# Kernel optimization log

Hardware: AMD Instinct MI355X
Metric: run time of the kernel (lower is better)

Reference implementation:

```python
import jax, jax.numpy as jnp
import numpy as np

IN_C, OUT_C = 64, 64
M1, M2 = 64, 64
H, W = 512, 512


def setup_inputs() -> dict:
    key = jax.random.key(0)
    ks = jax.random.split(key, 6)
    scale = 1.0 / (IN_C * M1 * M2) ** 0.5
    x = jax.random.normal(ks[0], (IN_C, H, W), dtype=jnp.float32)
    w_real = scale * jax.random.normal(ks[1], (IN_C, OUT_C, M1, M2), dtype=jnp.float32)
    w_imag = scale * jax.random.normal(ks[2], (IN_C, OUT_C, M1, M2), dtype=jnp.float32)
    b_conv = 0.01 * jax.random.normal(ks[3], (OUT_C,), dtype=jnp.float32)
    w_skip = (1.0 / IN_C ** 0.5) * jax.random.normal(ks[4], (OUT_C, IN_C), dtype=jnp.float32)
    b_skip = 0.01 * jax.random.normal(ks[5], (OUT_C,), dtype=jnp.float32)
    return {"x": x, "w_real": w_real, "w_imag": w_imag, "b_conv": b_conv,
            "w_skip": w_skip, "b_skip": b_skip}


def reference(x, w_real, w_imag, b_conv, w_skip, b_skip):
    # --- spectral convolution branch ---
    xf = jnp.fft.rfftn(x, axes=(1, 2))              # (in, H, W//2+1) complex
    xs = xf[:, :M1, :M2]                            # keep low modes (corner truncation)
    w = w_real + 1j * w_imag                        # (in, out, M1, M2)
    yf = jnp.einsum('ixy,ioxy->oxy', xs, w)         # complex mode mixing
    out_f = jnp.zeros((OUT_C, H, W // 2 + 1), dtype=yf.dtype).at[:, :M1, :M2].set(yf)
    conv = jnp.fft.irfftn(out_f, s=(H, W), axes=(1, 2)) + b_conv[:, None, None]
    # --- pointwise linear skip ---
    skip = jnp.einsum('oi,ixy->oxy', w_skip, x) + b_skip[:, None, None]
    # --- fuse and activate ---
    return jax.nn.gelu(conv + skip)
```

## Files before the change

kernel.cpp:

```cpp
#include <hip/hip_runtime.h>


using bf16x8 = __attribute__((ext_vector_type(8))) short;
using f32x4  = __attribute__((ext_vector_type(4))) float;
typedef unsigned short u16;

__device__ __forceinline__ u16 f2bf(float f) {
  unsigned u = __float_as_uint(f);
  u = u + 0x7FFFu + ((u >> 16) & 1u);
  return (u16)(u >> 16);
}
__device__ __forceinline__ float bf2f(u16 v) {
  return __uint_as_float(((unsigned)v) << 16);
}
__device__ __forceinline__ float rdx(const void* p, size_t i, int f32) {
  return f32 ? ((const float*)p)[i] : bf2f(((const u16*)p)[i]);
}

__global__ void sniff(const unsigned* __restrict__ xw, int* __restrict__ flag) {
  unsigned u = xw[threadIdx.x];
  int e = (u >> 7) & 0xFF;
  unsigned long long m = __ballot(e >= 110 && e <= 130);
  if (threadIdx.x == 0) *flag = (__popcll(m) < 32) ? 1 : 0;
}

__global__ __launch_bounds__(256) void init_tables(
    const void* __restrict__ wskip, const void* __restrict__ bconv,
    const void* __restrict__ bskip, const int* __restrict__ flag,
    u16* __restrict__ EW,
    u16* __restrict__ Gi,
    u16* __restrict__ Ct,
    u16* __restrict__ wbf,
    float* __restrict__ bias) {
  const int f32 = *flag;
  int t = blockIdx.x * blockDim.x + threadIdx.x;
  {
    int m = t >> 9, n = t & 511;
    int f = m >> 1, part = m & 1;
    int idx = (f * n) & 511;
    float ang = 0.01227184630308513f * (float)idx;
    float s, c; __sincosf(ang, &s, &c);
    EW[t] = f2bf(part ? -s : c);
  }
  {
    int h = t >> 7, cc = t & 127;
    int f = cc >> 1, part = cc & 1;
    int idx = (f * h) & 511;
    float ang = 0.01227184630308513f * (float)idx;
    float s, c; __sincosf(ang, &s, &c);
    Gi[t] = f2bf((part ? -s : c) * (1.0f / 512.0f));
    float scale = (f == 0 ? 1.0f : 2.0f) * (1.0f / 512.0f);
    Ct[t] = f2bf((part ? -s : c) * scale);
  }
  if (t < 4096) wbf[t] = f2bf(rdx(wskip, t, f32));
  if (t < 64) bias[t] = rdx(bconv, t, f32) + rdx(bskip, t, f32);
}

__global__ __launch_bounds__(256) void gemm_bt_x(
    const u16* __restrict__ A,  int lda,
    const void* __restrict__ BtV, int ldb, long long sB,
    u16* __restrict__ C,        int ldc, long long sC,
    int K, const int* __restrict__ flag) {
  const int f32 = *flag;
  const float* BtF = (const float*)BtV + (long long)blockIdx.z * sB;
  const u16*   BtH = (const u16*)BtV + (long long)blockIdx.z * sB;
  const int m0 = blockIdx.y * 64, n0 = blockIdx.x * 64;
  __shared__ __align__(16) u16 As[64][72];
  __shared__ __align__(16) u16 Bs[64][72];
  const int tid  = threadIdx.x;
  const int lane = tid & 63, wave = tid >> 6;
  const int srow = tid >> 2, sseg = (tid & 3) * 8;
  const int mb = (wave & 1) * 32, nb = (wave >> 1) * 32;
  const int fr = lane & 15, koff = (lane >> 4) * 8;
  f32x4 z = {0.f, 0.f, 0.f, 0.f};
  f32x4 acc00 = z, acc01 = z, acc10 = z, acc11 = z;
  for (int k0 = 0; k0 < K; k0 += 32) {
    __syncthreads();
    *(uint4*)&As[srow][sseg] = *(const uint4*)&A[(size_t)(m0 + srow) * lda + k0 + sseg];
    size_t bofs = (size_t)(n0 + srow) * ldb + k0 + sseg;
    if (f32) {
      float4 u = *(const float4*)(BtF + bofs);
      float4 v = *(const float4*)(BtF + bofs + 4);
      uint4 w;
      w.x = (unsigned)f2bf(u.x) | ((unsigned)f2bf(u.y) << 16);
      w.y = (unsigned)f2bf(u.z) | ((unsigned)f2bf(u.w) << 16);
      w.z = (unsigned)f2bf(v.x) | ((unsigned)f2bf(v.y) << 16);
      w.w = (unsigned)f2bf(v.z) | ((unsigned)f2bf(v.w) << 16);
      *(uint4*)&Bs[srow][sseg] = w;
    } else {
      *(uint4*)&Bs[srow][sseg] = *(const uint4*)(BtH + bofs);
    }
    __syncthreads();
    bf16x8 a0 = *(const bf16x8*)&As[mb + fr][koff];
    bf16x8 a1 = *(const bf16x8*)&As[mb + 16 + fr][koff];
    bf16x8 b0 = *(const bf16x8*)&Bs[nb + fr][koff];
    bf16x8 b1 = *(const bf16x8*)&Bs[nb + 16 + fr][koff];
    acc00 = __builtin_amdgcn_mfma_f32_16x16x32_bf16(a0, b0, acc00, 0, 0, 0);
    acc01 = __builtin_amdgcn_mfma_f32_16x16x32_bf16(a0, b1, acc01, 0, 0, 0);
    acc10 = __builtin_amdgcn_mfma_f32_16x16x32_bf16(a1, b0, acc10, 0, 0, 0);
    acc11 = __builtin_amdgcn_mfma_f32_16x16x32_bf16(a1, b1, acc11, 0, 0, 0);
  }
  const int col = lane & 15, rb = (lane >> 4) * 4;
  f32x4 accs[2][2] = {{acc00, acc01}, {acc10, acc11}};
  for (int mt = 0; mt < 2; ++mt)
    for (int nt = 0; nt < 2; ++nt)
      for (int r = 0; r < 4; ++r) {
        int mrow = m0 + mb + mt * 16 + rb + r;
        int ncol = n0 + nb + nt * 16 + col;
        C[(size_t)mrow * ldc + ncol] = f2bf(accs[mt][nt][r]);
      }
}

__global__ __launch_bounds__(256) void gemm_bt(
    const u16* __restrict__ A,  int lda, long long sA,
    const u16* __restrict__ Bt, int ldb, long long sB,
    u16* __restrict__ C,        int ldc, long long sC,
    int K) {
  A  += (long long)blockIdx.z * sA;
  Bt += (long long)blockIdx.z * sB;
  C  += (long long)blockIdx.z * sC;
  const int m0 = blockIdx.y * 64, n0 = blockIdx.x * 64;
  __shared__ __align__(16) u16 As[64][72];
  __shared__ __align__(16) u16 Bs[64][72];
  const int tid  = threadIdx.x;
  const int lane = tid & 63, wave = tid >> 6;
  const int srow = tid >> 2, sseg = (tid & 3) * 8;
  const int mb = (wave & 1) * 32, nb = (wave >> 1) * 32;
  const int fr = lane & 15, koff = (lane >> 4) * 8;
  f32x4 z = {0.f, 0.f, 0.f, 0.f};
  f32x4 acc00 = z, acc01 = z, acc10 = z, acc11 = z;
  for (int k0 = 0; k0 < K; k0 += 32) {
    __syncthreads();
    *(uint4*)&As[srow][sseg] = *(const uint4*)&A[(size_t)(m0 + srow) * lda + k0 + sseg];
    *(uint4*)&Bs[srow][sseg] = *(const uint4*)&Bt[(size_t)(n0 + srow) * ldb + k0 + sseg];
    __syncthreads();
    bf16x8 a0 = *(const bf16x8*)&As[mb + fr][koff];
    bf16x8 a1 = *(const bf16x8*)&As[mb + 16 + fr][koff];
    bf16x8 b0 = *(const bf16x8*)&Bs[nb + fr][koff];
    bf16x8 b1 = *(const bf16x8*)&Bs[nb + 16 + fr][koff];
    acc00 = __builtin_amdgcn_mfma_f32_16x16x32_bf16(a0, b0, acc00, 0, 0, 0);
    acc01 = __builtin_amdgcn_mfma_f32_16x16x32_bf16(a0, b1, acc01, 0, 0, 0);
    acc10 = __builtin_amdgcn_mfma_f32_16x16x32_bf16(a1, b0, acc10, 0, 0, 0);
    acc11 = __builtin_amdgcn_mfma_f32_16x16x32_bf16(a1, b1, acc11, 0, 0, 0);
  }
  const int col = lane & 15, rb = (lane >> 4) * 4;
  f32x4 accs[2][2] = {{acc00, acc01}, {acc10, acc11}};
  for (int mt = 0; mt < 2; ++mt)
    for (int nt = 0; nt < 2; ++nt)
      for (int r = 0; r < 4; ++r) {
        int mrow = m0 + mb + mt * 16 + rb + r;
        int ncol = n0 + nb + nt * 16 + col;
        C[(size_t)mrow * ldc + ncol] = f2bf(accs[mt][nt][r]);
      }
}

__global__ __launch_bounds__(256) void modemix(
    const u16* __restrict__ P, const void* __restrict__ wre,
    const void* __restrict__ wim, u16* __restrict__ yt,
    const int* __restrict__ flag) {
  const int f32 = *flag;
  const int o = blockIdx.x >> 4;
  const int kxg = blockIdx.x & 15;
  const int tid = threadIdx.x;
  const int ky = tid & 63;
  const int kxj = tid >> 6;
  const int kx = kxg * 4 + kxj;
  float yR = 0.f, yI = 0.f;
  for (int i = 0; i < 64; ++i) {
    const u16* prow = P + i * 16384 + (2 * kx) * 128 + 2 * ky;
    unsigned p0 = *(const unsigned*)prow;
    unsigned p1 = *(const unsigned*)(prow + 128);
    float p00 = bf2f((u16)(p0 & 0xFFFF)), p01 = bf2f((u16)(p0 >> 16));
    float p10 = bf2f((u16)(p1 & 0xFFFF)), p11 = bf2f((u16)(p1 >> 16));
    float xr = p00 - p11;
    float xi = p01 + p10;
    size_t widx = ((size_t)(i * 64 + o) * 64 + kx) * 64 + ky;
    float wr = rdx(wre, widx, f32);
    float wq = rdx(wim, widx, f32);
    yR += xr * wr - xi * wq;
    yI += xr * wq + xi * wr;
  }
  __shared__ u16 T[128][12];
  T[2 * ky][2 * kxj]         = f2bf(yR);
  T[2 * ky][2 * kxj + 1]     = f2bf(yI);
  T[2 * ky + 1][2 * kxj]     = f2bf(yI);
  T[2 * ky + 1][2 * kxj + 1] = f2bf(-yR);
  __syncthreads();
  int r = tid >> 1, s = (tid & 1) * 4;
  u16* dst = yt + (size_t)o * 16384 + (size_t)r * 128 + kxg * 8 + s;
  ushort4 v;
  v.x = T[r][s]; v.y = T[r][s + 1]; v.z = T[r][s + 2]; v.w = T[r][s + 3];
  *(ushort4*)dst = v;
}

__global__ __launch_bounds__(256) void inv_conv(
    const u16* __restrict__ Gi, const u16* __restrict__ Ct,
    const u16* __restrict__ yt, void* __restrict__ convV,
    const int* __restrict__ flag) {
  const int f32 = *flag;
  float* convF = (float*)convV;
  u16*   convH = (u16*)convV;
  const int m0 = blockIdx.x * 64;
  const int o  = blockIdx.y;
  __shared__ __align__(16) u16 lds[26112];
  u16* As = lds;
  u16* Bs = lds + 8704;
  const int tid = threadIdx.x, lane = tid & 63, wave = tid >> 6;
  const int fr = lane & 15, koff = (lane >> 4) * 8;
  const int col = lane & 15, rb = (lane >> 4) * 4;
  {
    int r = tid >> 2, cs = (tid & 3) * 32;
    const u16* g = Gi + (size_t)(m0 + r) * 128 + cs;
    u16* d = As + r * 136 + cs;
#pragma unroll
    for (int j = 0; j < 4; ++j) *(uint4*)(d + 8 * j) = *(const uint4*)(g + 8 * j);
  }
  {
    int r = tid >> 1, cs = (tid & 1) * 64;
    const u16* g = yt + (size_t)o * 16384 + (size_t)r * 128 + cs;
    u16* d = Bs + r * 136 + cs;
#pragma unroll
    for (int j = 0; j < 8; ++j) *(uint4*)(d + 8 * j) = *(const uint4*)(g + 8 * j);
  }
  __syncthreads();
  const int mb = (wave & 1) * 32, nh = (wave >> 1) * 64;
  f32x4 z = {0.f, 0.f, 0.f, 0.f};
  f32x4 acc1[2][4];
#pragma unroll
  for (int mt = 0; mt < 2; ++mt)
#pragma unroll
    for (int nt = 0; nt < 4; ++nt) acc1[mt][nt] = z;
  for (int k0 = 0; k0 < 128; k0 += 32) {
    bf16x8 a0 = *(const bf16x8*)(As + (mb + fr) * 136 + k0 + koff);
    bf16x8 a1 = *(const bf16x8*)(As + (mb + 16 + fr) * 136 + k0 + koff);
#pragma unroll
    for (int nt = 0; nt < 4; ++nt) {
      bf16x8 b = *(const bf16x8*)(Bs + (nh + nt * 16 + fr) * 136 + k0 + koff);
      acc1[0][nt] = __builtin_amdgcn_mfma_f32_16x16x32_bf16(a0, b, acc1[0][nt], 0, 0, 0);
      acc1[1][nt] = __builtin_amdgcn_mfma_f32_16x16x32_bf16(a1, b, acc1[1][nt], 0, 0, 0);
    }
  }
  __syncthreads();
  u16* T = Bs;
#pragma unroll
  for (int mt = 0; mt < 2; ++mt)
#pragma unroll
    for (int nt = 0; nt < 4; ++nt)
#pragma unroll
      for (int r = 0; r < 4; ++r)
        T[(mb + mt * 16 + rb + r) * 136 + nh + nt * 16 + col] = f2bf(acc1[mt][nt][r]);
  u16* Cs = lds;
  const int mb2 = (wave & 1) * 32, nb2 = (wave >> 1) * 32;
  for (int nb0 = 0; nb0 < 8; ++nb0) {
    __syncthreads();
    {
      int r = tid >> 2, cs = (tid & 3) * 32;
      const u16* g = Ct + (size_t)(nb0 * 64 + r) * 128 + cs;
      u16* d = Cs + r * 136 + cs;
#pragma unroll
      for (int j = 0; j < 4; ++j) *(uint4*)(d + 8 * j) = *(const uint4*)(g + 8 * j);
    }
    __syncthreads();
    f32x4 acc2[2][2] = {{z, z}, {z, z}};
    for (int k0 = 0; k0 < 128; k0 += 32) {
      bf16x8 a0 = *(const bf16x8*)(T + (mb2 + fr) * 136 + k0 + koff);
      bf16x8 a1 = *(const bf16x8*)(T + (mb2 + 16 + fr) * 136 + k0 + koff);
      bf16x8 b0 = *(const bf16x8*)(Cs + (nb2 + fr) * 136 + k0 + koff);
      bf16x8 b1 = *(const bf16x8*)(Cs + (nb2 + 16 + fr) * 136 + k0 + koff);
      acc2[0][0] = __builtin_amdgcn_mfma_f32_16x16x32_bf16(a0, b0, acc2[0][0], 0, 0, 0);
      acc2[0][1] = __builtin_amdgcn_mfma_f32_16x16x32_bf16(a0, b1, acc2[0][1], 0, 0, 0);
      acc2[1][0] = __builtin_amdgcn_mfma_f32_16x16x32_bf16(a1, b0, acc2[1][0], 0, 0, 0);
      acc2[1][1] = __builtin_amdgcn_mfma_f32_16x16x32_bf16(a1, b1, acc2[1][1], 0, 0, 0);
    }
#pragma unroll
    for (int mt = 0; mt < 2; ++mt)
#pragma unroll
      for (int nt = 0; nt < 2; ++nt)
#pragma unroll
        for (int r = 0; r < 4; ++r) {
          size_t idx = (size_t)o * 262144 + (size_t)(m0 + mb2 + mt * 16 + rb + r) * 512
                     + nb0 * 64 + nb2 + nt * 16 + col;
          float v = acc2[mt][nt][r];
          if (f32) convF[idx] = v; else convH[idx] = f2bf(v);
        }
  }
}

__global__ __launch_bounds__(256) void skip_final_mfma(
    const void* __restrict__ x, const u16* __restrict__ wbf,
    const float* __restrict__ bias, void* __restrict__ outV,
    const int* __restrict__ flag) {
  const int f32 = *flag;
  float* outF = (float*)outV;
  u16*   outH = (u16*)outV;
  const size_t p0 = (size_t)blockIdx.x * 128;
  __shared__ __align__(16) u16 As[64][72];
  __shared__ __align__(16) u16 Bs[128][72];
  const int tid = threadIdx.x, lane = tid & 63, wave = tid >> 6;
  {
    int r = tid >> 2, c0 = (tid & 3) * 16;
    *(uint4*)&As[r][c0]     = *(const uint4*)&wbf[r * 64 + c0];
    *(uint4*)&As[r][c0 + 8] = *(const uint4*)&wbf[r * 64 + c0 + 8];
  }
  {
    const int cq = tid >> 4;
    const int pq = tid & 15;
    const int c0 = cq * 4;
    for (int ib = 0; ib < 2; ++ib) {
      const int px = ib * 64 + pq * 4;
      u16 v[4][4];
      if (f32) {
        const float* xp = (const float*)x + p0 + px;
#pragma unroll
        for (int j = 0; j < 4; ++j) {
          float4 t = *(const float4*)(xp + (size_t)(c0 + j) * 262144);
          v[j][0] = f2bf(t.x); v[j][1] = f2bf(t.y);
          v[j][2] = f2bf(t.z); v[j][3] = f2bf(t.w);
        }
      } else {
        const u16* xp = (const u16*)x + p0 + px;
#pragma unroll
        for (int j = 0; j < 4; ++j) {
          ushort4 t = *(const ushort4*)(xp + (size_t)(c0 + j) * 262144);
          v[j][0] = t.x; v[j][1] = t.y; v[j][2] = t.z; v[j][3] = t.w;
        }
      }
#pragma unroll
      for (int k = 0; k < 4; ++k) {
        int row = px + k;
        int cs = c0 ^ (((row >> 2) & 7) << 3);
        ushort4 w4;
        w4.x = v[0][k]; w4.y = v[1][k]; w4.z = v[2][k]; w4.w = v[3][k];
        *(ushort4*)&Bs[row][cs] = w4;
      }
    }
  }
  __syncthreads();
  const int fr = lane & 15, koff = (lane >> 4) * 8;
  f32x4 z = {0.f, 0.f, 0.f, 0.f};
  f32x4 acc[4][2];
#pragma unroll
  for (int mi = 0; mi < 4; ++mi)
#pragma unroll
    for (int ni = 0; ni < 2; ++ni) acc[mi][ni] = z;
#pragma unroll
  for (int k0 = 0; k0 < 64; k0 += 32) {
    bf16x8 a[4], b[2];
#pragma unroll
    for (int mi = 0; mi < 4; ++mi)
      a[mi] = *(const bf16x8*)&As[mi * 16 + fr][k0 + koff];
#pragma unroll
    for (int ni = 0; ni < 2; ++ni) {
      int prow = wave * 32 + ni * 16 + fr;
      int sw = ((prow >> 2) & 7) << 3;
      b[ni] = *(const bf16x8*)&Bs[prow][(k0 + koff) ^ sw];
    }
#pragma unroll
    for (int mi = 0; mi < 4; ++mi)
#pragma unroll
      for (int ni = 0; ni < 2; ++ni)
        acc[mi][ni] = __builtin_amdgcn_mfma_f32_16x16x32_bf16(a[mi], b[ni], acc[mi][ni], 0, 0, 0);
  }
  const int col = lane & 15, rb = (lane >> 4) * 4;
#pragma unroll
  for (int mi = 0; mi < 4; ++mi)
#pragma unroll
    for (int ni = 0; ni < 2; ++ni)
#pragma unroll
      for (int r = 0; r < 4; ++r) {
        int o = mi * 16 + rb + r;
        size_t idx = (size_t)o * 262144 + p0 + wave * 32 + ni * 16 + col;
        float cv = f32 ? outF[idx] : bf2f(outH[idx]);
        float v = acc[mi][ni][r] + cv + bias[o];
        float zz = 1.5957691216f * (v + 0.044715f * v * v * v);
        float g = v / (1.f + __expf(-zz));
        if (f32) outF[idx] = g; else outH[idx] = f2bf(g);
      }
}

extern "C" void kernel_launch(void* const* d_in, const int* in_sizes, int n_in,
                              void* d_out, int out_size, void* d_ws, size_t ws_size,
                              hipStream_t stream) {
  const void* x     = d_in[0];
  const void* wre   = d_in[1];
  const void* wim   = d_in[2];
  const void* bconv = d_in[3];
  const void* wskip = d_in[4];
  const void* bskip = d_in[5];
  char* ws = (char*)d_ws;

  u16*   EW   = (u16*)(ws);
  u16*   Gi   = (u16*)(ws + (1 << 17));
  u16*   Ct   = (u16*)(ws + (2 << 17));
  u16*   wbf  = (u16*)(ws + 3 * (1 << 17));
  float* bias = (float*)(ws + 3 * (1 << 17) + 16384);
  int*   flag = (int*)(ws + 3 * (1 << 17) + 16640);
  u16*   yt   = (u16*)(ws + (1 << 19));
  u16* t1T = (u16*)d_out;
  u16* P   = (u16*)((char*)d_out + (8 << 20));

  sniff<<<1, 64, 0, stream>>>((const unsigned*)x, flag);
  init_tables<<<256, 256, 0, stream>>>(wskip, bconv, bskip, flag, EW, Gi, Ct, wbf, bias);
  gemm_bt_x<<<dim3(8, 2, 64), 256, 0, stream>>>(EW, 512, x, 512, 262144, t1T, 512, 65536, 512, flag);
  gemm_bt<<<dim3(2, 2, 64), 256, 0, stream>>>(EW, 512, 0, t1T, 512, 65536, P, 128, 16384, 512);
  modemix<<<1024, 256, 0, stream>>>(P, wre, wim, yt, flag);
  inv_conv<<<dim3(8, 64), 256, 0, stream>>>(Gi, Ct, yt, d_out, flag);
  skip_final_mfma<<<2048, 256, 0, stream>>>(x, wbf, bias, d_out, flag);
}
```

Measured before the change: 301.6 us.

## Cover full M per block in forward DFT GEMM; read skip weights from global

The first DFT GEMM now uses 512-thread blocks that cover all 128 output rows at once. Each block therefore loads and converts every fp32 tile of x only once, instead of once for each of two M-blocks, which halves the dominant input read traffic. The output pointer now also advances per batch slice via sC, which the old kernel never did. In the skip kernel, the shared-memory staging of the 64x64 skip weights is dropped; the MFMA operands are read straight from global and cache, with an occupancy hint of 6 blocks. The risks are lower occupancy with the larger blocks and uncoalesced or cache-dependent weight loads in the skip kernel.

```diff
diff --git a/kernel.cpp b/kernel.cpp
--- a/kernel.cpp
+++ b/kernel.cpp
@@ -56,7 +56,7 @@
   if (t < 64) bias[t] = rdx(bconv, t, f32) + rdx(bskip, t, f32);
 }
 
-__global__ __launch_bounds__(256) void gemm_bt_x(
+__global__ __launch_bounds__(512) void gemm_bt_x(
     const u16* __restrict__ A,  int lda,
     const void* __restrict__ BtV, int ldb, long long sB,
     u16* __restrict__ C,        int ldc, long long sC,
@@ -64,31 +64,29 @@
   const int f32 = *flag;
   const float* BtF = (const float*)BtV + (long long)blockIdx.z * sB;
   const u16*   BtH = (const u16*)BtV + (long long)blockIdx.z * sB;
-  const int m0 = blockIdx.y * 64, n0 = blockIdx.x * 64;
-  __shared__ __align__(16) u16 As[64][72];
+  C += (long long)blockIdx.z * sC;
+  const int n0 = blockIdx.x * 64;
+  __shared__ __align__(16) u16 As[128][72];
   __shared__ __align__(16) u16 Bs[64][72];
   const int tid  = threadIdx.x;
   const int lane = tid & 63, wave = tid >> 6;
-  const int srow = tid >> 2, sseg = (tid & 3) * 8;
-  const int mb = (wave & 1) * 32, nb = (wave >> 1) * 32;
+  const int srowA = tid >> 2, ssegA = (tid & 3) * 8;
+  const int srowB = tid >> 3, ssegB = (tid & 7) * 4;
+  const int mb = (wave & 3) * 32, nb = (wave >> 2) * 32;
   const int fr = lane & 15, koff = (lane >> 4) * 8;
   f32x4 z = {0.f, 0.f, 0.f, 0.f};
   f32x4 acc00 = z, acc01 = z, acc10 = z, acc11 = z;
   for (int k0 = 0; k0 < K; k0 += 32) {
     __syncthreads();
-    *(uint4*)&As[srow][sseg] = *(const uint4*)&A[(size_t)(m0 + srow) * lda + k0 + sseg];
-    size_t bofs = (size_t)(n0 + srow) * ldb + k0 + sseg;
+    *(uint4*)&As[srowA][ssegA] = *(const uint4*)&A[(size_t)srowA * lda + k0 + ssegA];
+    size_t bofs = (size_t)(n0 + srowB) * ldb + k0 + ssegB;
     if (f32) {
       float4 u = *(const float4*)(BtF + bofs);
-      float4 v = *(const float4*)(BtF + bofs + 4);
-      uint4 w;
-      w.x = (unsigned)f2bf(u.x) | ((unsigned)f2bf(u.y) << 16);
-      w.y = (unsigned)f2bf(u.z) | ((unsigned)f2bf(u.w) << 16);
-      w.z = (unsigned)f2bf(v.x) | ((unsigned)f2bf(v.y) << 16);
-      w.w = (unsigned)f2bf(v.z) | ((unsigned)f2bf(v.w) << 16);
-      *(uint4*)&Bs[srow][sseg] = w;
+      ushort4 w;
+      w.x = f2bf(u.x); w.y = f2bf(u.y); w.z = f2bf(u.z); w.w = f2bf(u.w);
+      *(ushort4*)&Bs[srowB][ssegB] = w;
     } else {
-      *(uint4*)&Bs[srow][sseg] = *(const uint4*)(BtH + bofs);
+      *(ushort4*)&Bs[srowB][ssegB] = *(const ushort4*)(BtH + bofs);
     }
     __syncthreads();
     bf16x8 a0 = *(const bf16x8*)&As[mb + fr][koff];
@@ -105,7 +103,7 @@
   for (int mt = 0; mt < 2; ++mt)
     for (int nt = 0; nt < 2; ++nt)
       for (int r = 0; r < 4; ++r) {
-        int mrow = m0 + mb + mt * 16 + rb + r;
+        int mrow = mb + mt * 16 + rb + r;
         int ncol = n0 + nb + nt * 16 + col;
         C[(size_t)mrow * ldc + ncol] = f2bf(accs[mt][nt][r]);
       }
@@ -286,7 +284,7 @@
   }
 }
 
-__global__ __launch_bounds__(256) void skip_final_mfma(
+__global__ __launch_bounds__(256, 6) void skip_final_mfma(
     const void* __restrict__ x, const u16* __restrict__ wbf,
     const float* __restrict__ bias, void* __restrict__ outV,
     const int* __restrict__ flag) {
@@ -294,14 +292,8 @@
   float* outF = (float*)outV;
   u16*   outH = (u16*)outV;
   const size_t p0 = (size_t)blockIdx.x * 128;
-  __shared__ __align__(16) u16 As[64][72];
   __shared__ __align__(16) u16 Bs[128][72];
   const int tid = threadIdx.x, lane = tid & 63, wave = tid >> 6;
-  {
-    int r = tid >> 2, c0 = (tid & 3) * 16;
-    *(uint4*)&As[r][c0]     = *(const uint4*)&wbf[r * 64 + c0];
-    *(uint4*)&As[r][c0 + 8] = *(const uint4*)&wbf[r * 64 + c0 + 8];
-  }
   {
     const int cq = tid >> 4;
     const int pq = tid & 15;
@@ -348,7 +340,7 @@
     bf16x8 a[4], b[2];
 #pragma unroll
     for (int mi = 0; mi < 4; ++mi)
-      a[mi] = *(const bf16x8*)&As[mi * 16 + fr][k0 + koff];
+      a[mi] = *(const bf16x8*)&wbf[(size_t)(mi * 16 + fr) * 64 + k0 + koff];
 #pragma unroll
     for (int ni = 0; ni < 2; ++ni) {
       int prow = wave * 32 + ni * 16 + fr;
@@ -401,7 +393,7 @@
 
   sniff<<<1, 64, 0, stream>>>((const unsigned*)x, flag);
   init_tables<<<256, 256, 0, stream>>>(wskip, bconv, bskip, flag, EW, Gi, Ct, wbf, bias);
-  gemm_bt_x<<<dim3(8, 2, 64), 256, 0, stream>>>(EW, 512, x, 512, 262144, t1T, 512, 65536, 512, flag);
+  gemm_bt_x<<<dim3(8, 1, 64), 512, 0, stream>>>(EW, 512, x, 512, 262144, t1T, 512, 65536, 512, flag);
   gemm_bt<<<dim3(2, 2, 64), 256, 0, stream>>>(EW, 512, 0, t1T, 512, 65536, P, 128, 16384, 512);
   modemix<<<1024, 256, 0, stream>>>(P, wre, wim, yt, flag);
   inv_conv<<<dim3(8, 64), 256, 0, stream>>>(Gi, Ct, yt, d_out, flag);
```

Result: no change. 299.6 us (-0.7%).
